# Optimization experiments

Measured on AMD Instinct MI355X. Metric: run time of the kernel, lower is better.

## Reference

```python
import jax, jax.numpy as jnp
import numpy as np

ALPHA = 0.2        # LeakyReLU negative slope
NEG_BIG = -9e15    # mask fill value from the original module


def setup_inputs() -> dict:
    key = jax.random.key(0)
    k1, k2, k3, k4 = jax.random.split(key, 4)
    B, N, F_in, F_out = 4, 4096, 128, 64
    h = jax.random.normal(k1, (B, N, F_in), dtype=jnp.float32)
    adj = jax.random.randint(k2, (N, N), 0, 2, dtype=jnp.int32)
    W = jax.random.normal(k3, (F_in, F_out), dtype=jnp.float32)
    a = jax.random.normal(k4, (2 * F_out, 1), dtype=jnp.float32)
    return {"h": h, "adj": adj, "W": W, "a": a}


def reference(h, adj, W, a):
    # h: [B, N, F_in], adj: [N, N], W: [F_in, F_out], a: [2*F_out, 1]
    F_out = W.shape[1]
    hW = jnp.einsum('bni,io->bno', h, W)               # [B, N, F_out]
    f1 = hW @ a[:F_out, :]                             # [B, N, 1]
    f2 = hW @ a[F_out:, :]                             # [B, N, 1]
    e = f1 + jnp.swapaxes(f2, 1, 2)                    # [B, N, N] broadcast-add
    e = jax.nn.leaky_relu(e, negative_slope=ALPHA)
    e = jax.nn.softmax(e, axis=2)
    # dropout is a no-op (is_training=False)
    attention = jnp.where(adj[None, :, :] > 0, e, NEG_BIG)
    new_h = jax.nn.sigmoid(jnp.einsum('bnm,bmo->bno', attention, hW))
    return new_h
```

## Files before the change

kernel.cpp:

```cpp
#include <hip/hip_runtime.h>
#include <hip/hip_bf16.h>


#define GN 4096
#define GB 4
#define FIN 128
#define FOUT 64

typedef int i32x4 __attribute__((ext_vector_type(4)));
typedef unsigned int uint32x4 __attribute__((ext_vector_type(4)));
typedef float f32x4 __attribute__((ext_vector_type(4)));

__global__ __launch_bounds__(256) void front_kernel(const int* __restrict__ adj,
                                                    const float* __restrict__ h,
                                                    const float* __restrict__ W,
                                                    unsigned long long* __restrict__ tmask,
                                                    double* __restrict__ hW,
                                                    unsigned char* __restrict__ Bp) {
    __shared__ float hs[4][FIN];
    __shared__ unsigned int dg[4][64];

    if (blockIdx.x < 1024) {
        int wid = blockIdx.x * 4 + (threadIdx.x >> 6);
        int lane = threadIdx.x & 63;
        int rt = wid >> 6, s = wid & 63;
        int row16 = lane & 15, g = lane >> 4;
        const int* base = adj + (size_t)(rt * 64 + row16) * GN + s * 64 + g * 16;
        unsigned long long res = 0ull;
#pragma unroll
        for (int r = 0; r < 4; ++r) {
            const i32x4* p = (const i32x4*)(base + (size_t)r * 16 * GN);
            unsigned int b16 = 0;
#pragma unroll
            for (int q = 0; q < 4; ++q) {
                i32x4 v = p[q];
                b16 |= (v.x == 0 ? 1u : 0u) << (q * 4);
                b16 |= (v.y == 0 ? 2u : 0u) << (q * 4);
                b16 |= (v.z == 0 ? 4u : 0u) << (q * 4);
                b16 |= (v.w == 0 ? 8u : 0u) << (q * 4);
            }
            res |= (unsigned long long)b16 << (r * 16);
        }
        tmask[(size_t)wid * 64 + lane] = res;
    } else {
        const int bx = blockIdx.x - 1024;
        const int grp = threadIdx.x >> 6;
        const int o = threadIdx.x & 63;
        const int b = bx >> 10, q4 = bx & 1023;
        {
            const f32x4* src = (const f32x4*)(h + ((size_t)b * GN + q4 * 4) * FIN);
            f32x4* dst = (f32x4*)&hs[0][0];
            if (threadIdx.x < 128) dst[threadIdx.x] = src[threadIdx.x];
        }
        __syncthreads();
        double a0 = 0, a1 = 0, a2 = 0, a3 = 0;
#pragma unroll
        for (int i = 0; i < FIN; i += 4) {
            a0 = fma((double)hs[grp][i],     (double)W[i * FOUT + o],       a0);
            a1 = fma((double)hs[grp][i + 1], (double)W[(i + 1) * FOUT + o], a1);
            a2 = fma((double)hs[grp][i + 2], (double)W[(i + 2) * FOUT + o], a2);
            a3 = fma((double)hs[grp][i + 3], (double)W[(i + 3) * FOUT + o], a3);
        }
        double acc = (a0 + a1) + (a2 + a3);
        hW[((size_t)b * GN + q4 * 4 + grp) * FOUT + o] = acc;

        int qi = (int)llrint(acc * 65536.0);
        int d0 = ((qi + 128) & 255) - 128; qi = (qi - d0) >> 8;
        int d1 = ((qi + 128) & 255) - 128; qi = (qi - d1) >> 8;
        dg[grp][o] = (unsigned int)(d0 & 255) | ((unsigned int)(d1 & 255) << 8)
                   | ((unsigned int)(qi & 255) << 16);
        __syncthreads();
        if (grp < 3) {
            unsigned int w = 0;
#pragma unroll
            for (int rr = 0; rr < 4; ++rr)
                w |= ((dg[rr][o] >> (grp * 8)) & 255u) << (rr * 8);
            const int p = q4 >> 4, g = (q4 >> 2) & 3, qr = q4 & 3;
            const int cg = o >> 4, col16 = o & 15;
            *(unsigned int*)(Bp + ((size_t)b * 64 + p) * 12288 + grp * 4096
                             + cg * 1024 + g * 256 + col16 * 16 + qr * 4) = w;
        }
    }
}

__global__ __launch_bounds__(512, 1) void gemm_kernel(const unsigned char* __restrict__ Bp,
                                                      const unsigned long long* __restrict__ tmask,
                                                      const double* __restrict__ hW,
                                                      float* __restrict__ out) {
    __shared__ __align__(16) unsigned char lds[49152];
    __shared__ unsigned int nflag;
    __shared__ unsigned int flagbuf[128];
    __shared__ double fred[8];

    const int tid = threadIdx.x, lane = tid & 63, wv = tid >> 6;
    const int cg = wv & 3, kg = wv >> 2;
    const int rt = (int)blockIdx.x >> 2, b = (int)blockIdx.x & 3;
    if (tid == 0) nflag = 0;

    const unsigned char* bptr = Bp + (size_t)b * 786432 + kg * 12288 + cg * 1024 + lane * 16;
    const unsigned long long* mptr = tmask + (size_t)rt * 4096 + kg * 64 + lane;

    i32x4 acc[4][3];
#pragma unroll
    for (int r = 0; r < 4; ++r)
#pragma unroll
        for (int pl = 0; pl < 3; ++pl) {
            i32x4 z = {0, 0, 0, 0};
            acc[r][pl] = z;
        }

    i32x4 ba0 = *(const i32x4*)(bptr);
    i32x4 ba1 = *(const i32x4*)(bptr + 4096);
    i32x4 ba2 = *(const i32x4*)(bptr + 8192);
    unsigned long long ma = mptr[0];
    i32x4 bb0 = *(const i32x4*)(bptr + 24576);
    i32x4 bb1 = *(const i32x4*)(bptr + 24576 + 4096);
    i32x4 bb2 = *(const i32x4*)(bptr + 24576 + 8192);
    unsigned long long mb = mptr[128];

    auto dostep = [&](unsigned long long mw, i32x4 v0, i32x4 v1, i32x4 v2) {
        const unsigned int mlo = (unsigned int)mw, mhi = (unsigned int)(mw >> 32);
#pragma unroll
        for (int r = 0; r < 4; ++r) {
            unsigned int half = (r >> 1) ? mhi : mlo;
            unsigned int w16 = (r & 1) ? (half >> 16) : (half & 0xFFFFu);
            uint32x4 u;
#pragma unroll
            for (int q = 0; q < 4; ++q)
                u[q] = (((w16 >> (4 * q)) & 0xFu) * 0x00204081u) & 0x01010101u;
            i32x4 af = __builtin_bit_cast(i32x4, u);
            acc[r][0] = __builtin_amdgcn_mfma_i32_16x16x64_i8(af, v0, acc[r][0], 0, 0, 0);
            acc[r][1] = __builtin_amdgcn_mfma_i32_16x16x64_i8(af, v1, acc[r][1], 0, 0, 0);
            acc[r][2] = __builtin_amdgcn_mfma_i32_16x16x64_i8(af, v2, acc[r][2], 0, 0, 0);
        }
    };

    for (int T = 0; T < 32; T += 2) {
        dostep(ma, ba0, ba1, ba2);
        if (T + 2 < 32) {
            const unsigned char* g2 = bptr + (size_t)(T + 2) * 24576;
            ba0 = *(const i32x4*)(g2);
            ba1 = *(const i32x4*)(g2 + 4096);
            ba2 = *(const i32x4*)(g2 + 8192);
            ma = mptr[(size_t)(T + 2) * 128];
        }
        dostep(mb, bb0, bb1, bb2);
        if (T + 3 < 32) {
            const unsigned char* g3 = bptr + (size_t)(T + 3) * 24576;
            bb0 = *(const i32x4*)(g3);
            bb1 = *(const i32x4*)(g3 + 4096);
            bb2 = *(const i32x4*)(g3 + 8192);
            mb = mptr[(size_t)(T + 3) * 128];
        }
    }

    __syncthreads();
    if (kg == 1) {
        unsigned char* dst = lds + cg * 12288 + lane * 192;
#pragma unroll
        for (int r = 0; r < 4; ++r)
#pragma unroll
            for (int pl = 0; pl < 3; ++pl)
                *(i32x4*)(dst + (r * 3 + pl) * 16) = acc[r][pl];
    }
    __syncthreads();
    if (kg == 0) {
        const unsigned char* s2 = lds + cg * 12288 + lane * 192;
#pragma unroll
        for (int r = 0; r < 4; ++r)
#pragma unroll
            for (int pl = 0; pl < 3; ++pl) {
                i32x4 v = *(const i32x4*)(s2 + (r * 3 + pl) * 16);
#pragma unroll
                for (int q = 0; q < 4; ++q) acc[r][pl][q] += v[q];
            }

        const int o = cg * 16 + (lane & 15);
#pragma unroll
        for (int r = 0; r < 4; ++r) {
#pragma unroll
            for (int q = 0; q < 4; ++q) {
                double S = (double)acc[r][0][q] + 256.0 * (double)acc[r][1][q]
                         + 65536.0 * (double)acc[r][2][q];
                int i = rt * 64 + r * 16 + (lane >> 4) * 4 + q;
                size_t oi = ((size_t)b * GN + i) * FOUT + o;
                out[oi] = S < 0.0 ? 1.0f : 0.0f;
                if (fabs(S) <= 2048.0) {
                    unsigned int idx = atomicAdd(&nflag, 1u);
                    if (idx < 128) flagbuf[idx] = ((unsigned int)i << 6) | (unsigned int)o;
                }
            }
        }
    }

    __syncthreads();
    unsigned int nf = nflag;
    if (nf > 128) nf = 128;
    for (unsigned int f = 0; f < nf; ++f) {
        unsigned int e = flagbuf[f];
        int o = e & 63;
        int i = (int)(e >> 6);
        int row16 = i & 15, r = (i >> 4) & 3;
        int s = tid >> 3, lg = (tid >> 1) & 3, hf = tid & 1;
        unsigned long long w = tmask[((size_t)rt * 64 + s) * 64 + (lg * 16 + row16)];
        double ps = 0.0;
        const double* hwc = hW + ((size_t)b * GN + s * 64 + lg * 16) * FOUT + o;
#pragma unroll
        for (int jj = hf * 8; jj < hf * 8 + 8; ++jj) {
            if ((w >> (r * 16 + jj)) & 1ull)
                ps += hwc[(size_t)jj * FOUT];
        }
#pragma unroll
        for (int d = 32; d >= 1; d >>= 1) ps += __shfl_down(ps, d, 64);
        if (lane == 0) fred[wv] = ps;
        __syncthreads();
        if (tid == 0) {
            double tot = ((fred[0] + fred[1]) + (fred[2] + fred[3]))
                       + ((fred[4] + fred[5]) + (fred[6] + fred[7]));
            out[((size_t)b * GN + i) * FOUT + o] = tot < 0.0 ? 1.0f : 0.0f;
        }
        __syncthreads();
    }
}

extern "C" void kernel_launch(void* const* d_in, const int* in_sizes, int n_in,
                              void* d_out, int out_size, void* d_ws, size_t ws_size,
                              hipStream_t stream) {
    const float* h   = (const float*)d_in[0];
    const int*   adj = (const int*)d_in[1];
    const float* W   = (const float*)d_in[2];
    float* out = (float*)d_out;

    char* ws = (char*)d_ws;
    double* hW                = (double*)ws;
    unsigned char* Bp         = (unsigned char*)(ws + 8388608);
    unsigned long long* tmask = (unsigned long long*)(ws + 12582912);

    front_kernel<<<5120, 256, 0, stream>>>(adj, h, W, tmask, hW, Bp);
    gemm_kernel<<<256, 512, 0, stream>>>(Bp, tmask, hW, out);
}
```

Baseline: 61.79 us.

## Split front kernel, coalesce adjacency packing via LDS, remap GEMM blocks per XCD

Splits the fused front kernel into a separate adjacency-packing kernel and an hW/repack kernel. The packing kernel now has each thread read contiguous chunks of one adjacency row and transposes the 16-bit masks through shared memory, giving more coalesced reads of the 64MB adj matrix. The GEMM block index is remapped so blocks on the same XCD share a batch and a contiguous row-tile range, aiming for better L2 reuse of Bp. This adds one extra kernel launch, and the packing stage now runs with only 256 blocks, which may underfill the GPU.

```diff
diff --git a/kernel.cpp b/kernel.cpp
--- a/kernel.cpp
+++ b/kernel.cpp
@@ -11,75 +11,85 @@
 typedef unsigned int uint32x4 __attribute__((ext_vector_type(4)));
 typedef float f32x4 __attribute__((ext_vector_type(4)));
 
-__global__ __launch_bounds__(256) void front_kernel(const int* __restrict__ adj,
-                                                    const float* __restrict__ h,
-                                                    const float* __restrict__ W,
-                                                    unsigned long long* __restrict__ tmask,
-                                                    double* __restrict__ hW,
-                                                    unsigned char* __restrict__ Bp) {
+__global__ __launch_bounds__(256) void pack_kernel(const int* __restrict__ adj,
+                                                   unsigned long long* __restrict__ tmask) {
+    __shared__ unsigned short m16[64][68];
+    const int t = threadIdx.x;
+    const int rt = (int)blockIdx.x >> 2, cp = (int)blockIdx.x & 3;
+
+    const int row = t >> 2, jq = t & 3;
+    const int* rbase = adj + (size_t)(rt * 64 + row) * GN + cp * 1024;
+#pragma unroll
+    for (int it = 0; it < 16; ++it) {
+        const int j16 = it * 4 + jq;
+        const i32x4* p = (const i32x4*)(rbase + j16 * 16);
+        unsigned int b16 = 0;
+#pragma unroll
+        for (int q = 0; q < 4; ++q) {
+            i32x4 v = p[q];
+            b16 |= (v.x == 0 ? 1u : 0u) << (q * 4);
+            b16 |= (v.y == 0 ? 2u : 0u) << (q * 4);
+            b16 |= (v.z == 0 ? 4u : 0u) << (q * 4);
+            b16 |= (v.w == 0 ? 8u : 0u) << (q * 4);
+        }
+        m16[row][j16] = (unsigned short)b16;
+    }
+    __syncthreads();
+
+#pragma unroll
+    for (int it = 0; it < 4; ++it) {
+        const int idx = it * 256 + t;
+        const int sloc = idx >> 6, l = idx & 63;
+        const int row16 = l & 15, g = l >> 4;
+        unsigned long long res = 0ull;
+#pragma unroll
+        for (int r = 0; r < 4; ++r)
+            res |= (unsigned long long)m16[r * 16 + row16][sloc * 4 + g] << (r * 16);
+        tmask[((size_t)rt * 64 + cp * 16 + sloc) * 64 + l] = res;
+    }
+}
+
+__global__ __launch_bounds__(256) void hwrepack_kernel(const float* __restrict__ h,
+                                                       const float* __restrict__ W,
+                                                       double* __restrict__ hW,
+                                                       unsigned char* __restrict__ Bp) {
+    const int grp = threadIdx.x >> 6;
+    const int o = threadIdx.x & 63;
+    const int b = (int)blockIdx.x >> 10, q4 = (int)blockIdx.x & 1023;
     __shared__ float hs[4][FIN];
     __shared__ unsigned int dg[4][64];
-
-    if (blockIdx.x < 1024) {
-        int wid = blockIdx.x * 4 + (threadIdx.x >> 6);
-        int lane = threadIdx.x & 63;
-        int rt = wid >> 6, s = wid & 63;
-        int row16 = lane & 15, g = lane >> 4;
-        const int* base = adj + (size_t)(rt * 64 + row16) * GN + s * 64 + g * 16;
-        unsigned long long res = 0ull;
-#pragma unroll
-        for (int r = 0; r < 4; ++r) {
-            const i32x4* p = (const i32x4*)(base + (size_t)r * 16 * GN);
-            unsigned int b16 = 0;
-#pragma unroll
-            for (int q = 0; q < 4; ++q) {
-                i32x4 v = p[q];
-                b16 |= (v.x == 0 ? 1u : 0u) << (q * 4);
-                b16 |= (v.y == 0 ? 2u : 0u) << (q * 4);
-                b16 |= (v.z == 0 ? 4u : 0u) << (q * 4);
-                b16 |= (v.w == 0 ? 8u : 0u) << (q * 4);
-            }
-            res |= (unsigned long long)b16 << (r * 16);
-        }
-        tmask[(size_t)wid * 64 + lane] = res;
-    } else {
-        const int bx = blockIdx.x - 1024;
-        const int grp = threadIdx.x >> 6;
-        const int o = threadIdx.x & 63;
-        const int b = bx >> 10, q4 = bx & 1023;
-        {
-            const f32x4* src = (const f32x4*)(h + ((size_t)b * GN + q4 * 4) * FIN);
-            f32x4* dst = (f32x4*)&hs[0][0];
-            if (threadIdx.x < 128) dst[threadIdx.x] = src[threadIdx.x];
-        }
-        __syncthreads();
-        double a0 = 0, a1 = 0, a2 = 0, a3 = 0;
-#pragma unroll
-        for (int i = 0; i < FIN; i += 4) {
-            a0 = fma((double)hs[grp][i],     (double)W[i * FOUT + o],       a0);
-            a1 = fma((double)hs[grp][i + 1], (double)W[(i + 1) * FOUT + o], a1);
-            a2 = fma((double)hs[grp][i + 2], (double)W[(i + 2) * FOUT + o], a2);
-            a3 = fma((double)hs[grp][i + 3], (double)W[(i + 3) * FOUT + o], a3);
-        }
-        double acc = (a0 + a1) + (a2 + a3);
-        hW[((size_t)b * GN + q4 * 4 + grp) * FOUT + o] = acc;
-
-        int qi = (int)llrint(acc * 65536.0);
-        int d0 = ((qi + 128) & 255) - 128; qi = (qi - d0) >> 8;
-        int d1 = ((qi + 128) & 255) - 128; qi = (qi - d1) >> 8;
-        dg[grp][o] = (unsigned int)(d0 & 255) | ((unsigned int)(d1 & 255) << 8)
-                   | ((unsigned int)(qi & 255) << 16);
-        __syncthreads();
-        if (grp < 3) {
-            unsigned int w = 0;
-#pragma unroll
-            for (int rr = 0; rr < 4; ++rr)
-                w |= ((dg[rr][o] >> (grp * 8)) & 255u) << (rr * 8);
-            const int p = q4 >> 4, g = (q4 >> 2) & 3, qr = q4 & 3;
-            const int cg = o >> 4, col16 = o & 15;
-            *(unsigned int*)(Bp + ((size_t)b * 64 + p) * 12288 + grp * 4096
-                             + cg * 1024 + g * 256 + col16 * 16 + qr * 4) = w;
-        }
+    {
+        const f32x4* src = (const f32x4*)(h + ((size_t)b * GN + q4 * 4) * FIN);
+        f32x4* dst = (f32x4*)&hs[0][0];
+        if (threadIdx.x < 128) dst[threadIdx.x] = src[threadIdx.x];
+    }
+    __syncthreads();
+    double a0 = 0, a1 = 0, a2 = 0, a3 = 0;
+#pragma unroll
+    for (int i = 0; i < FIN; i += 4) {
+        a0 = fma((double)hs[grp][i],     (double)W[i * FOUT + o],       a0);
+        a1 = fma((double)hs[grp][i + 1], (double)W[(i + 1) * FOUT + o], a1);
+        a2 = fma((double)hs[grp][i + 2], (double)W[(i + 2) * FOUT + o], a2);
+        a3 = fma((double)hs[grp][i + 3], (double)W[(i + 3) * FOUT + o], a3);
+    }
+    double acc = (a0 + a1) + (a2 + a3);
+    hW[((size_t)b * GN + q4 * 4 + grp) * FOUT + o] = acc;
+
+    int qi = (int)llrint(acc * 65536.0);
+    int d0 = ((qi + 128) & 255) - 128; qi = (qi - d0) >> 8;
+    int d1 = ((qi + 128) & 255) - 128; qi = (qi - d1) >> 8;
+    dg[grp][o] = (unsigned int)(d0 & 255) | ((unsigned int)(d1 & 255) << 8)
+               | ((unsigned int)(qi & 255) << 16);
+    __syncthreads();
+    if (grp < 3) {
+        unsigned int w = 0;
+#pragma unroll
+        for (int rr = 0; rr < 4; ++rr)
+            w |= ((dg[rr][o] >> (grp * 8)) & 255u) << (rr * 8);
+        const int p = q4 >> 4, g = (q4 >> 2) & 3, qr = q4 & 3;
+        const int cg = o >> 4, col16 = o & 15;
+        *(unsigned int*)(Bp + ((size_t)b * 64 + p) * 12288 + grp * 4096
+                         + cg * 1024 + g * 256 + col16 * 16 + qr * 4) = w;
     }
 }
 
@@ -94,7 +104,8 @@
 
     const int tid = threadIdx.x, lane = tid & 63, wv = tid >> 6;
     const int cg = wv & 3, kg = wv >> 2;
-    const int rt = (int)blockIdx.x >> 2, b = (int)blockIdx.x & 3;
+    const int xcd = (int)blockIdx.x & 7, wslot = (int)blockIdx.x >> 3;
+    const int b = xcd >> 1, rt = (xcd & 1) * 32 + wslot;
     if (tid == 0) nflag = 0;
 
     const unsigned char* bptr = Bp + (size_t)b * 786432 + kg * 12288 + cg * 1024 + lane * 16;
@@ -236,6 +247,7 @@
     unsigned char* Bp         = (unsigned char*)(ws + 8388608);
     unsigned long long* tmask = (unsigned long long*)(ws + 12582912);
 
-    front_kernel<<<5120, 256, 0, stream>>>(adj, h, W, tmask, hW, Bp);
+    pack_kernel<<<256, 256, 0, stream>>>(adj, tmask);
+    hwrepack_kernel<<<4096, 256, 0, stream>>>(h, W, hW, Bp);
     gemm_kernel<<<256, 512, 0, stream>>>(Bp, tmask, hW, out);
 }
```

Measured after the change: 64.24 us. 4.0% more time.
